# Performance work log

Hardware: AMD Instinct MI355X
Metric: run time of the kernel (lower is better)

The kernel has to match this reference:

```python
import jax, jax.numpy as jnp
import numpy as np

N = 8192
F_IN = 256
F_OUT = 256
S = 128          # state_dim
D_INNER = 512    # int(2.0 * out_features)


def _ln(x, g, b, eps=1e-5):
    m = x.mean(-1, keepdims=True)
    v = ((x - m) ** 2).mean(-1, keepdims=True)
    return (x - m) / jnp.sqrt(v + eps) * g + b


def setup_inputs() -> dict:
    key = jax.random.key(0)
    ks = jax.random.split(key, 20)
    s = 0.05
    d = {}
    d['h'] = jax.random.normal(ks[0], (N, F_IN), dtype=jnp.float32)
    d['adj'] = jax.random.randint(ks[1], (N, N), 0, 2, dtype=jnp.int32)
    d['W'] = jax.random.normal(ks[2], (F_IN, F_OUT), dtype=jnp.float32) * s
    d['a_src'] = jax.random.normal(ks[3], (F_OUT, 1), dtype=jnp.float32) * s
    d['a_dst'] = jax.random.normal(ks[4], (F_OUT, 1), dtype=jnp.float32) * s
    d['W_bcdt'] = jax.random.normal(ks[5], (F_OUT, 3 * S), dtype=jnp.float32) * s
    d['b_bcdt'] = jnp.zeros((3 * S,), jnp.float32)
    d['abp_w'] = jax.random.normal(ks[6], (S, F_OUT), dtype=jnp.float32) * s
    d['abp_b'] = jnp.zeros((F_OUT,), jnp.float32)
    d['cp_w'] = jax.random.normal(ks[7], (S, 1), dtype=jnp.float32) * s
    d['cp_b'] = jnp.zeros((1,), jnp.float32)
    d['W_hz'] = jax.random.normal(ks[8], (F_OUT, 2 * D_INNER), dtype=jnp.float32) * s
    d['b_hz'] = jnp.zeros((2 * D_INNER,), jnp.float32)
    d['out_w'] = jax.random.normal(ks[9], (D_INNER, F_OUT), dtype=jnp.float32) * s
    d['out_b'] = jnp.zeros((F_OUT,), jnp.float32)
    d['fe1_w'] = jax.random.normal(ks[10], (F_OUT, D_INNER), dtype=jnp.float32) * s
    d['fe1_b'] = jnp.zeros((D_INNER,), jnp.float32)
    d['fe_ln_g'] = jnp.ones((D_INNER,), jnp.float32)
    d['fe_ln_b'] = jnp.zeros((D_INNER,), jnp.float32)
    d['fe2_w'] = jax.random.normal(ks[11], (D_INNER, F_OUT), dtype=jnp.float32) * s
    d['fe2_b'] = jnp.zeros((F_OUT,), jnp.float32)
    d['A'] = jax.random.uniform(ks[12], (S,), minval=1.0, maxval=64.0, dtype=jnp.float32)
    d['D'] = jnp.ones((1,), jnp.float32)
    d['g1_w'] = jax.random.normal(ks[13], (2 * F_OUT, 2 * F_OUT), dtype=jnp.float32) * s
    d['g1_b'] = jnp.zeros((2 * F_OUT,), jnp.float32)
    d['g_ln_g'] = jnp.ones((2 * F_OUT,), jnp.float32)
    d['g_ln_b'] = jnp.zeros((2 * F_OUT,), jnp.float32)
    d['g2_w'] = jax.random.normal(ks[14], (2 * F_OUT, F_OUT), dtype=jnp.float32) * s
    d['g2_b'] = jnp.zeros((F_OUT,), jnp.float32)
    d['ln_g'] = jnp.ones((F_OUT,), jnp.float32)
    d['ln_b'] = jnp.zeros((F_OUT,), jnp.float32)
    return d


def reference(h, adj, W, a_src, a_dst, W_bcdt, b_bcdt, abp_w, abp_b, cp_w, cp_b,
              W_hz, b_hz, out_w, out_b, fe1_w, fe1_b, fe_ln_g, fe_ln_b, fe2_w,
              fe2_b, A, D, g1_w, g1_b, g_ln_g, g_ln_b, g2_w, g2_b, ln_g, ln_b):
    Wh = h @ W                                   # [N, F_OUT]
    # GAT-style masked attention
    e = Wh @ a_src + (Wh @ a_dst).T              # [N, N]
    e = jnp.where(e > 0, e, 0.2 * e)             # leaky_relu(0.2)
    e = jnp.where(adj > 0, e, jnp.float32(-9e15))
    attn = jax.nn.softmax(e, axis=1)
    h_attn = attn @ Wh                           # [N, F_OUT]
    # feature enhancer
    h_enh = jax.nn.silu(_ln(Wh @ fe1_w + fe1_b, fe_ln_g, fe_ln_b)) @ fe2_w + fe2_b
    # SSM-like branch
    BCdt = Wh @ W_bcdt + b_bcdt                  # [N, 3S]
    B, C, dt = jnp.split(BCdt, 3, axis=1)
    Asm = jax.nn.softmax(dt + A[None, :], axis=1)
    ab = (Asm * B) @ abp_w + abp_b               # [N, F_OUT]
    hs = Wh * ab
    hz = hs @ W_hz + b_hz                        # [N, 2*D_INNER]
    h_part, z = jnp.split(hz, 2, axis=1)
    hs = (h_part * jax.nn.silu(z) + h_part * D) @ out_w + out_b
    c_proj = C @ cp_w + cp_b                     # [N, 1]
    hs = hs * (1.0 + c_proj)
    # gated fusion
    comb = jnp.concatenate([h_attn, hs], axis=1)  # [N, 2*F_OUT]
    g = jax.nn.sigmoid(jax.nn.silu(_ln(comb @ g1_w + g1_b, g_ln_g, g_ln_b)) @ g2_w + g2_b)
    fused = g * h_attn + (1.0 - g) * hs + h_enh
    return _ln(fused, ln_g, ln_b)
```

## Files before the change

kernel.cpp:

```cpp
#include <hip/hip_runtime.h>
#include <cstdint>

typedef __attribute__((ext_vector_type(8))) short short8;
typedef __attribute__((ext_vector_type(4))) float f32x4;

#define DEVINL static __device__ __forceinline__

DEVINL ushort f2b(float f) {
    uint32_t u = __builtin_bit_cast(uint32_t, f);
    u += 0x7FFFu + ((u >> 16) & 1u);
    return (ushort)(u >> 16);
}

typedef __attribute__((address_space(3))) uint32_t lds_u32;
typedef const __attribute__((address_space(1))) uint32_t glb_u32;

DEVINL void load_lds_16(const ushort* g, ushort* l) {
    __builtin_amdgcn_global_load_lds((glb_u32*)g, (lds_u32*)l, 16, 0, 0);
}

constexpr int EPI_F32      = 0;
constexpr int EPI_MUL_BF16 = 2;
constexpr int EPI_SCALE_FB = 3;
constexpr int EPI_WH       = 4;

template<int K, int EPI>
__global__ __launch_bounds__(256) void gemm_k(
    const ushort* __restrict__ A, const ushort* __restrict__ BT,
    const float* __restrict__ bias, int N,
    float* __restrict__ outf, ushort* __restrict__ outb, int obld, int oboff,
    const float* __restrict__ extra,
    const float* __restrict__ asrc, const float* __restrict__ adst,
    float* __restrict__ sOut, float* __restrict__ dOut)
{
    __shared__ ushort Asm[128 * 64];
    __shared__ ushort Bsm[64 * 64];

    const int wave = threadIdx.x >> 6;
    const int lane = threadIdx.x & 63;
    const int quad = lane >> 4;
    const int l16  = lane & 15;
    const int lr   = lane >> 3, ls = lane & 7;
    const int m0 = blockIdx.x * 128;
    const int n0 = blockIdx.y * 64;

    f32x4 zero = {0.f, 0.f, 0.f, 0.f};
    f32x4 acc[2][4] = {{zero, zero, zero, zero}, {zero, zero, zero, zero}};

    for (int k0 = 0; k0 < K; k0 += 64) {
        #pragma unroll
        for (int p = 0; p < 4; ++p) {
            const int r = wave * 32 + p * 8 + lr;
            load_lds_16(A + (size_t)(m0 + r) * K + k0 + ((ls ^ (r & 7)) * 8),
                        Asm + (size_t)(wave * 32 + p * 8) * 64);
        }
        #pragma unroll
        for (int p = 0; p < 2; ++p) {
            const int n = wave * 16 + p * 8 + lr;
            load_lds_16(BT + (size_t)(n0 + n) * K + k0 + ((ls ^ (n & 7)) * 8),
                        Bsm + (size_t)(wave * 16 + p * 8) * 64);
        }
        __syncthreads();
        #pragma unroll
        for (int ks = 0; ks < 2; ++ks) {
            const int kg = ks * 4 + quad;
            const int sl = (kg ^ (l16 & 7)) * 8;
            short8 a0 = *(const short8*)(Asm + (wave * 32 + l16) * 64 + sl);
            short8 a1 = *(const short8*)(Asm + (wave * 32 + 16 + l16) * 64 + sl);
            #pragma unroll
            for (int c = 0; c < 4; ++c) {
                short8 bf = *(const short8*)(Bsm + (c * 16 + l16) * 64 + sl);
                acc[0][c] = __builtin_amdgcn_mfma_f32_16x16x32_bf16(a0, bf, acc[0][c], 0, 0, 0);
                acc[1][c] = __builtin_amdgcn_mfma_f32_16x16x32_bf16(a1, bf, acc[1][c], 0, 0, 0);
            }
        }
        __syncthreads();
    }

    #pragma unroll
    for (int it = 0; it < 2; ++it) {
        #pragma unroll
        for (int r = 0; r < 4; ++r) {
            const int row = m0 + wave * 32 + it * 16 + quad * 4 + r;
            float sp = 0.f, dp = 0.f;
            #pragma unroll
            for (int c = 0; c < 4; ++c) {
                const int col = n0 + c * 16 + l16;
                float v = acc[it][c][r] + (bias ? bias[col] : 0.f);
                if (EPI == EPI_MUL_BF16) v *= extra[(size_t)row * N + col];
                if (EPI == EPI_SCALE_FB) v *= extra[row];
                if (EPI == EPI_F32 || EPI == EPI_SCALE_FB || EPI == EPI_WH)
                    outf[(size_t)row * N + col] = v;
                if (EPI == EPI_MUL_BF16 || EPI == EPI_SCALE_FB || EPI == EPI_WH)
                    outb[(size_t)row * obld + oboff + col] = f2b(v);
                if (EPI == EPI_WH) { sp += v * asrc[col]; dp += v * adst[col]; }
            }
            if (EPI == EPI_WH) {
                #pragma unroll
                for (int o = 1; o < 16; o <<= 1) {
                    sp += __shfl_xor(sp, o);
                    dp += __shfl_xor(dp, o);
                }
                if (l16 == 0) {
                    atomicAdd(&sOut[row], sp);
                    atomicAdd(&dOut[row], dp);
                }
            }
        }
    }
}

__global__ __launch_bounds__(256) void attn_kernel(
    const int* __restrict__ adj, const float* __restrict__ sA,
    const float* __restrict__ dA, const ushort* __restrict__ WhT,
    float* __restrict__ Upart, float* __restrict__ lpart)
{
    __shared__ ushort vsm[256 * 64];
    __shared__ ushort wsm[64 * 64];

    const int tid  = threadIdx.x;
    const int wave = tid >> 6, lane = tid & 63, quad = lane >> 4, l16 = lane & 15;
    const int lr = lane >> 3, ls = lane & 7;
    const int i0 = blockIdx.x * 64;
    const int js = blockIdx.y;
    const int jbase = js * 2048;
    const int pr = tid >> 2, pc = tid & 3;
    const float s_r = sA[i0 + pr];
    const int* adjp = adj + (size_t)(i0 + pr) * 8192 + jbase;
    const int rt = wave & 1, ch = wave >> 1;

    f32x4 zero = {0.f, 0.f, 0.f, 0.f};
    f32x4 acc[2][8] = {{zero, zero, zero, zero, zero, zero, zero, zero},
                       {zero, zero, zero, zero, zero, zero, zero, zero}};
    float lsum = 0.f;

    for (int c64 = 0; c64 < 2048; c64 += 64) {
        #pragma unroll
        for (int p = 0; p < 8; ++p) {
            const int f = wave * 64 + p * 8 + lr;
            load_lds_16(WhT + (size_t)f * 8192 + jbase + c64 + ((ls ^ (f & 7)) * 8),
                        vsm + (size_t)(wave * 64 + p * 8) * 64);
        }
        #pragma unroll
        for (int gi = 0; gi < 2; ++gi) {
            const int g = pc + gi * 4;
            const int4   a0 = *(const int4*)  (adjp + c64 + g * 8);
            const int4   a1 = *(const int4*)  (adjp + c64 + g * 8 + 4);
            const float4 d0 = *(const float4*)(dA + jbase + c64 + g * 8);
            const float4 d1 = *(const float4*)(dA + jbase + c64 + g * 8 + 4);
            const int   aa[8] = {a0.x, a0.y, a0.z, a0.w, a1.x, a1.y, a1.z, a1.w};
            const float dd[8] = {d0.x, d0.y, d0.z, d0.w, d1.x, d1.y, d1.z, d1.w};
            union { ushort us[8]; uint4 v; } pk;
            #pragma unroll
            for (int q = 0; q < 8; ++q) {
                float e = s_r + dd[q];
                e = fmaxf(e, 0.2f * e);
                const float w = aa[q] ? __expf(e) : 0.f;
                lsum += w; pk.us[q] = f2b(w);
            }
            *(uint4*)(wsm + pr * 64 + ((g ^ (pr & 7)) * 8)) = pk.v;
        }
        __syncthreads();

        #pragma unroll
        for (int ks = 0; ks < 2; ++ks) {
            const int kg = ks * 4 + quad;
            const int sl = (kg ^ (l16 & 7)) * 8;
            short8 a0 = *(const short8*)(wsm + (rt * 32 + l16) * 64 + sl);
            short8 a1 = *(const short8*)(wsm + (rt * 32 + 16 + l16) * 64 + sl);
            #pragma unroll
            for (int c = 0; c < 8; ++c) {
                short8 bf = *(const short8*)(vsm + (ch * 128 + c * 16 + l16) * 64 + sl);
                acc[0][c] = __builtin_amdgcn_mfma_f32_16x16x32_bf16(a0, bf, acc[0][c], 0, 0, 0);
                acc[1][c] = __builtin_amdgcn_mfma_f32_16x16x32_bf16(a1, bf, acc[1][c], 0, 0, 0);
            }
        }
        __syncthreads();
    }

    lsum += __shfl_down(lsum, 1);
    lsum += __shfl_down(lsum, 2);
    if (pc == 0) lpart[(size_t)js * 8192 + i0 + pr] = lsum;

    #pragma unroll
    for (int it = 0; it < 2; ++it) {
        #pragma unroll
        for (int c = 0; c < 8; ++c) {
            const int col = ch * 128 + c * 16 + l16;
            #pragma unroll
            for (int r = 0; r < 4; ++r) {
                const int row = i0 + rt * 32 + it * 16 + quad * 4 + r;
                Upart[((size_t)js * 8192 + row) * 256 + col] = acc[it][c][r];
            }
        }
    }
}

__global__ __launch_bounds__(256) void attn_combine_kernel(
    const float* __restrict__ Upart, const float* __restrict__ lpart,
    float* __restrict__ outf, ushort* __restrict__ outb)
{
    const int row = blockIdx.x * 4 + (threadIdx.x >> 6);
    const int lane = threadIdx.x & 63;
    float l = 0.f;
    #pragma unroll
    for (int js = 0; js < 4; ++js) l += lpart[(size_t)js * 8192 + row];
    const float inv = 1.f / l;
    #pragma unroll
    for (int i = 0; i < 4; ++i) {
        const int c = i * 64 + lane;
        float u = 0.f;
        #pragma unroll
        for (int js = 0; js < 4; ++js)
            u += Upart[((size_t)js * 8192 + row) * 256 + c];
        const float v = u * inv;
        outf[(size_t)row * 256 + c] = v;
        outb[(size_t)row * 512 + c] = f2b(v);
    }
}

struct TJob { const float* in; ushort* out; int R, C, off; };
struct TArgs { TJob j[10]; };

__global__ __launch_bounds__(256) void multi_transpose_kernel(TArgs a)
{
    __shared__ float tile[32][33];
    const int b = blockIdx.x;
    int ji = 0;
    #pragma unroll
    for (int k = 1; k < 10; ++k) if (b >= a.j[k].off) ji = k;
    const TJob J = a.j[ji];
    const int t = b - J.off;

    if (J.R == 0) {
        const int base = t * 1024 + threadIdx.x;
        #pragma unroll
        for (int k = 0; k < 4; ++k)
            J.out[base + k * 256] = f2b(J.in[base + k * 256]);
        return;
    }
    const int CB = J.C >> 5;
    const int bx = t % CB, by = t / CB;
    const int tx = threadIdx.x & 31, ty = threadIdx.x >> 5;
    const int c0 = bx * 32, r0 = by * 32;
    #pragma unroll
    for (int i = ty; i < 32; i += 8)
        tile[i][tx] = J.in[(size_t)(r0 + i) * J.C + (c0 + tx)];
    __syncthreads();
    #pragma unroll
    for (int i = ty; i < 32; i += 8)
        J.out[(size_t)(c0 + i) * J.R + (r0 + tx)] = f2b(tile[tx][i]);
}

__global__ __launch_bounds__(256) void transpose_cast_kernel(
    const float* __restrict__ in, ushort* __restrict__ out, int R, int C)
{
    __shared__ float tile[32][33];
    const int tx = threadIdx.x & 31, ty = threadIdx.x >> 5;
    const int c0 = blockIdx.x * 32, r0 = blockIdx.y * 32;
    #pragma unroll
    for (int i = ty; i < 32; i += 8)
        tile[i][tx] = in[(size_t)(r0 + i) * C + (c0 + tx)];
    __syncthreads();
    #pragma unroll
    for (int i = ty; i < 32; i += 8)
        out[(size_t)(c0 + i) * R + (r0 + tx)] = f2b(tile[tx][i]);
}

__global__ __launch_bounds__(256) void ln_silu_512_kernel(
    const float* __restrict__ in, const float* __restrict__ g,
    const float* __restrict__ b, ushort* __restrict__ outb)
{
    const int row = blockIdx.x * 4 + (threadIdx.x >> 6);
    const int lane = threadIdx.x & 63;
    const size_t base = (size_t)row * 512;
    float x[8]; float sum = 0.f, sq = 0.f;
    #pragma unroll
    for (int i = 0; i < 8; ++i) {
        const float v = in[base + i * 64 + lane];
        x[i] = v; sum += v; sq += v * v;
    }
    #pragma unroll
    for (int o = 32; o; o >>= 1) { sum += __shfl_xor(sum, o); sq += __shfl_xor(sq, o); }
    const float mean = sum * (1.f / 512.f);
    const float var  = sq * (1.f / 512.f) - mean * mean;
    const float rstd = rsqrtf(var + 1e-5f);
    #pragma unroll
    for (int i = 0; i < 8; ++i) {
        const int c = i * 64 + lane;
        const float y = (x[i] - mean) * rstd * g[c] + b[c];
        outb[base + c] = f2b(y / (1.f + __expf(-y)));
    }
}

__global__ __launch_bounds__(256) void ssm_front_kernel(
    const float* __restrict__ BCdt, const float* __restrict__ Avec,
    const float* __restrict__ cpw, const float* __restrict__ cpb,
    ushort* __restrict__ SB, float* __restrict__ cscale)
{
    const int row = blockIdx.x * 4 + (threadIdx.x >> 6);
    const int lane = threadIdx.x & 63;
    const float* rp = BCdt + (size_t)row * 384;
    const float B0 = rp[lane],       B1 = rp[64 + lane];
    const float C0 = rp[128 + lane], C1 = rp[192 + lane];
    float t0 = rp[256 + lane] + Avec[lane];
    float t1 = rp[320 + lane] + Avec[64 + lane];
    float mx = fmaxf(t0, t1);
    #pragma unroll
    for (int o = 32; o; o >>= 1) mx = fmaxf(mx, __shfl_xor(mx, o));
    const float e0 = __expf(t0 - mx), e1 = __expf(t1 - mx);
    float ssum = e0 + e1;
    #pragma unroll
    for (int o = 32; o; o >>= 1) ssum += __shfl_xor(ssum, o);
    const float inv = 1.f / ssum;
    SB[(size_t)row * 128 + lane]      = f2b(e0 * inv * B0);
    SB[(size_t)row * 128 + 64 + lane] = f2b(e1 * inv * B1);
    float cp = C0 * cpw[lane] + C1 * cpw[64 + lane];
    #pragma unroll
    for (int o = 32; o; o >>= 1) cp += __shfl_xor(cp, o);
    if (lane == 0) cscale[row] = 1.f + cp + cpb[0];
}

__global__ void hz_act_kernel(const float* __restrict__ hz,
                              const float* __restrict__ Dp, ushort* __restrict__ out)
{
    const float D0 = Dp[0];
    const int n = 8192 * 512;
    for (int i = blockIdx.x * blockDim.x + threadIdx.x; i < n; i += gridDim.x * blockDim.x) {
        const int r = i >> 9, c = i & 511;
        const float hp = hz[(size_t)r * 1024 + c];
        const float z  = hz[(size_t)r * 1024 + 512 + c];
        out[i] = f2b(hp * (z / (1.f + __expf(-z)) + D0));
    }
}

__global__ __launch_bounds__(256) void final_kernel(
    const float* __restrict__ gl, const float* __restrict__ ha,
    const float* __restrict__ hs2, const float* __restrict__ he,
    const float* __restrict__ lng, const float* __restrict__ lnb,
    float* __restrict__ outp)
{
    const int row = blockIdx.x * 4 + (threadIdx.x >> 6);
    const int lane = threadIdx.x & 63;
    const size_t base = (size_t)row * 256;
    float f[4]; float sum = 0.f, sq = 0.f;
    #pragma unroll
    for (int i = 0; i < 4; ++i) {
        const int c = i * 64 + lane;
        const float gv = 1.f / (1.f + __expf(-gl[base + c]));
        const float v = gv * ha[base + c] + (1.f - gv) * hs2[base + c] + he[base + c];
        f[i] = v; sum += v; sq += v * v;
    }
    #pragma unroll
    for (int o = 32; o; o >>= 1) { sum += __shfl_xor(sum, o); sq += __shfl_xor(sq, o); }
    const float mean = sum * (1.f / 256.f);
    const float var  = sq * (1.f / 256.f) - mean * mean;
    const float rstd = rsqrtf(var + 1e-5f);
    #pragma unroll
    for (int i = 0; i < 4; ++i) {
        const int c = i * 64 + lane;
        outp[base + c] = (f[i] - mean) * rstd * lng[c] + lnb[c];
    }
}

extern "C" void kernel_launch(void* const* d_in, const int* in_sizes, int n_in,
                              void* d_out, int out_size, void* d_ws, size_t ws_size,
                              hipStream_t stream)
{
    const float* h      = (const float*)d_in[0];
    const int*   adj    = (const int*)  d_in[1];
    const float* W      = (const float*)d_in[2];
    const float* a_src  = (const float*)d_in[3];
    const float* a_dst  = (const float*)d_in[4];
    const float* W_bcdt = (const float*)d_in[5];
    const float* b_bcdt = (const float*)d_in[6];
    const float* abp_w  = (const float*)d_in[7];
    const float* abp_b  = (const float*)d_in[8];
    const float* cp_w   = (const float*)d_in[9];
    const float* cp_b   = (const float*)d_in[10];
    const float* W_hz   = (const float*)d_in[11];
    const float* b_hz   = (const float*)d_in[12];
    const float* out_w  = (const float*)d_in[13];
    const float* out_b  = (const float*)d_in[14];
    const float* fe1_w  = (const float*)d_in[15];
    const float* fe1_b  = (const float*)d_in[16];
    const float* fe_ln_g= (const float*)d_in[17];
    const float* fe_ln_b= (const float*)d_in[18];
    const float* fe2_w  = (const float*)d_in[19];
    const float* fe2_b  = (const float*)d_in[20];
    const float* Avec   = (const float*)d_in[21];
    const float* Dvec   = (const float*)d_in[22];
    const float* g1_w   = (const float*)d_in[23];
    const float* g1_b   = (const float*)d_in[24];
    const float* g_ln_g = (const float*)d_in[25];
    const float* g_ln_b = (const float*)d_in[26];
    const float* g2_w   = (const float*)d_in[27];
    const float* g2_b   = (const float*)d_in[28];
    const float* ln_g   = (const float*)d_in[29];
    const float* ln_b   = (const float*)d_in[30];
    float* outp = (float*)d_out;

    char* p = (char*)d_ws;
    size_t off = 0;
    auto take = [&](size_t nbytes) -> void* {
        void* r = p + off;
        off += (nbytes + 255) & ~(size_t)255;
        return r;
    };
    ushort* wT    = (ushort*)take(256 * 256 * 2);
    ushort* fe1T  = (ushort*)take(512 * 256 * 2);
    ushort* fe2T  = (ushort*)take(256 * 512 * 2);
    ushort* bcdtT = (ushort*)take(384 * 256 * 2);
    ushort* abpT  = (ushort*)take(256 * 128 * 2);
    ushort* hzT   = (ushort*)take(1024 * 256 * 2);
    ushort* outT  = (ushort*)take(256 * 512 * 2);
    ushort* g1T   = (ushort*)take(512 * 512 * 2);
    ushort* g2T   = (ushort*)take(256 * 512 * 2);
    ushort* hbf   = (ushort*)take((size_t)8192 * 256 * 2);
    float*  Wh    = (float*) take((size_t)8192 * 256 * 4);
    ushort* Whbf  = (ushort*)take((size_t)8192 * 256 * 2);
    ushort* WhT   = (ushort*)take((size_t)8192 * 256 * 2);
    float*  sbuf  = (float*) take(8192 * 4);
    float*  dbuf  = (float*) take(8192 * 4);
    float*  cscl  = (float*) take(8192 * 4);
    float*  hattn = (float*) take((size_t)8192 * 256 * 4);
    float*  henh  = (float*) take((size_t)8192 * 256 * 4);
    float*  BCdt  = (float*) take((size_t)8192 * 384 * 4);
    ushort* SB    = (ushort*)take((size_t)8192 * 128 * 2);
    ushort* hsbf  = (ushort*)take((size_t)8192 * 256 * 2);
    ushort* vbf   = (ushort*)take((size_t)8192 * 512 * 2);
    float*  hs2   = (float*) take((size_t)8192 * 256 * 4);
    ushort* comb  = (ushort*)take((size_t)8192 * 512 * 2);
    ushort* tact  = (ushort*)take((size_t)8192 * 512 * 2);
    float*  big   = (float*) take((size_t)8192 * 1024 * 4);
    float*  gl    = BCdt;
    float*  Upart = big;
    float*  lpart = BCdt;

    (void)in_sizes; (void)n_in; (void)out_size; (void)ws_size;

    hipMemsetAsync(sbuf, 0, 2 * 8192 * sizeof(float), stream);

    {
        TArgs ta; int boff = 0;
        auto addT = [&](int i, const float* in, ushort* out, int R, int C) {
            ta.j[i] = TJob{in, out, R, C, boff};
            boff += (R / 32) * (C / 32);
        };
        addT(0, W,      wT,    256, 256);
        addT(1, fe1_w,  fe1T,  256, 512);
        addT(2, fe2_w,  fe2T,  512, 256);
        addT(3, W_bcdt, bcdtT, 256, 384);
        addT(4, abp_w,  abpT,  128, 256);
        addT(5, W_hz,   hzT,   256, 1024);
        addT(6, out_w,  outT,  512, 256);
        addT(7, g1_w,   g1T,   512, 512);
        addT(8, g2_w,   g2T,   512, 256);
        ta.j[9] = TJob{h, hbf, 0, 8192 * 256, boff};
        boff += (8192 * 256) / 1024;
        multi_transpose_kernel<<<boff, 256, 0, stream>>>(ta);
    }

    gemm_k<256, EPI_WH><<<dim3(64, 4), 256, 0, stream>>>(
        hbf, wT, nullptr, 256, Wh, Whbf, 256, 0, nullptr, a_src, a_dst, sbuf, dbuf);
    transpose_cast_kernel<<<dim3(8, 256), 256, 0, stream>>>(Wh, WhT, 8192, 256);

    attn_kernel<<<dim3(128, 4), 256, 0, stream>>>(adj, sbuf, dbuf, WhT, Upart, lpart);
    attn_combine_kernel<<<2048, 256, 0, stream>>>(Upart, lpart, hattn, comb);

    gemm_k<256, EPI_F32><<<dim3(64, 8), 256, 0, stream>>>(
        Whbf, fe1T, fe1_b, 512, big, nullptr, 0, 0, nullptr, nullptr, nullptr, nullptr, nullptr);
    ln_silu_512_kernel<<<2048, 256, 0, stream>>>(big, fe_ln_g, fe_ln_b, tact);
    gemm_k<512, EPI_F32><<<dim3(64, 4), 256, 0, stream>>>(
        tact, fe2T, fe2_b, 256, henh, nullptr, 0, 0, nullptr, nullptr, nullptr, nullptr, nullptr);

    gemm_k<256, EPI_F32><<<dim3(64, 6), 256, 0, stream>>>(
        Whbf, bcdtT, b_bcdt, 384, BCdt, nullptr, 0, 0, nullptr, nullptr, nullptr, nullptr, nullptr);
    ssm_front_kernel<<<2048, 256, 0, stream>>>(BCdt, Avec, cp_w, cp_b, SB, cscl);
    gemm_k<128, EPI_MUL_BF16><<<dim3(64, 4), 256, 0, stream>>>(
        SB, abpT, abp_b, 256, nullptr, hsbf, 256, 0, Wh, nullptr, nullptr, nullptr, nullptr);
    gemm_k<256, EPI_F32><<<dim3(64, 16), 256, 0, stream>>>(
        hsbf, hzT, b_hz, 1024, big, nullptr, 0, 0, nullptr, nullptr, nullptr, nullptr, nullptr);
    hz_act_kernel<<<4096, 256, 0, stream>>>(big, Dvec, vbf);
    gemm_k<512, EPI_SCALE_FB><<<dim3(64, 4), 256, 0, stream>>>(
        vbf, outT, out_b, 256, hs2, comb, 512, 256, cscl, nullptr, nullptr, nullptr, nullptr);

    gemm_k<512, EPI_F32><<<dim3(64, 8), 256, 0, stream>>>(
        comb, g1T, g1_b, 512, big, nullptr, 0, 0, nullptr, nullptr, nullptr, nullptr, nullptr);
    ln_silu_512_kernel<<<2048, 256, 0, stream>>>(big, g_ln_g, g_ln_b, tact);
    gemm_k<512, EPI_F32><<<dim3(64, 4), 256, 0, stream>>>(
        tact, g2T, g2_b, 256, gl, nullptr, 0, 0, nullptr, nullptr, nullptr, nullptr, nullptr);
    final_kernel<<<2048, 256, 0, stream>>>(gl, hattn, hs2, henh, ln_g, ln_b, outp);
}
```

Baseline: 645.9 us.

## Fuse row-wise epilogues (LN+SiLU, SSM softmax, hz gating, final LN) into GEMMs

Adds a full-row GEMM kernel with 16-row tiles spanning all output columns, so LayerNorm+SiLU, the SSM softmax/scale, the hz gating and the final gated-fusion LayerNorm run in the GEMM epilogue. This drops the separate elementwise kernels and the fp32 intermediate round trips through global memory. The W_hz weight columns are permuted during transpose so each block holds matching h and z halves. The generic GEMM tile is halved to 64x64 to double the grid. Small row tiles reload the whole B matrix per block and get less reuse, and the attention scratch buffers are now separately allocated.

```diff
diff --git a/kernel.cpp b/kernel.cpp
--- a/kernel.cpp
+++ b/kernel.cpp
@@ -33,78 +33,313 @@
     const float* __restrict__ asrc, const float* __restrict__ adst,
     float* __restrict__ sOut, float* __restrict__ dOut)
 {
-    __shared__ ushort Asm[128 * 64];
+    __shared__ ushort Asm[64 * 64];
     __shared__ ushort Bsm[64 * 64];
 
     const int wave = threadIdx.x >> 6;
     const int lane = threadIdx.x & 63;
-    const int quad = lane >> 4;
-    const int l16  = lane & 15;
-    const int lr   = lane >> 3, ls = lane & 7;
-    const int m0 = blockIdx.x * 128;
+    const int quad = lane >> 4, l16 = lane & 15;
+    const int lr = lane >> 3, ls = lane & 7;
+    const int m0 = blockIdx.x * 64;
     const int n0 = blockIdx.y * 64;
 
     f32x4 zero = {0.f, 0.f, 0.f, 0.f};
-    f32x4 acc[2][4] = {{zero, zero, zero, zero}, {zero, zero, zero, zero}};
+    f32x4 acc[4] = {zero, zero, zero, zero};
 
     for (int k0 = 0; k0 < K; k0 += 64) {
         #pragma unroll
-        for (int p = 0; p < 4; ++p) {
-            const int r = wave * 32 + p * 8 + lr;
+        for (int p = 0; p < 2; ++p) {
+            const int r = wave * 16 + p * 8 + lr;
             load_lds_16(A + (size_t)(m0 + r) * K + k0 + ((ls ^ (r & 7)) * 8),
-                        Asm + (size_t)(wave * 32 + p * 8) * 64);
-        }
-        #pragma unroll
-        for (int p = 0; p < 2; ++p) {
-            const int n = wave * 16 + p * 8 + lr;
-            load_lds_16(BT + (size_t)(n0 + n) * K + k0 + ((ls ^ (n & 7)) * 8),
+                        Asm + (size_t)(wave * 16 + p * 8) * 64);
+            load_lds_16(BT + (size_t)(n0 + r) * K + k0 + ((ls ^ (r & 7)) * 8),
                         Bsm + (size_t)(wave * 16 + p * 8) * 64);
         }
         __syncthreads();
         #pragma unroll
         for (int ks = 0; ks < 2; ++ks) {
-            const int kg = ks * 4 + quad;
-            const int sl = (kg ^ (l16 & 7)) * 8;
-            short8 a0 = *(const short8*)(Asm + (wave * 32 + l16) * 64 + sl);
-            short8 a1 = *(const short8*)(Asm + (wave * 32 + 16 + l16) * 64 + sl);
+            const int sl = ((ks * 4 + quad) ^ (l16 & 7)) * 8;
+            short8 af = *(const short8*)(Asm + (wave * 16 + l16) * 64 + sl);
             #pragma unroll
             for (int c = 0; c < 4; ++c) {
                 short8 bf = *(const short8*)(Bsm + (c * 16 + l16) * 64 + sl);
-                acc[0][c] = __builtin_amdgcn_mfma_f32_16x16x32_bf16(a0, bf, acc[0][c], 0, 0, 0);
-                acc[1][c] = __builtin_amdgcn_mfma_f32_16x16x32_bf16(a1, bf, acc[1][c], 0, 0, 0);
-            }
-        }
-        __syncthreads();
-    }
-
-    #pragma unroll
-    for (int it = 0; it < 2; ++it) {
-        #pragma unroll
-        for (int r = 0; r < 4; ++r) {
-            const int row = m0 + wave * 32 + it * 16 + quad * 4 + r;
-            float sp = 0.f, dp = 0.f;
-            #pragma unroll
-            for (int c = 0; c < 4; ++c) {
-                const int col = n0 + c * 16 + l16;
-                float v = acc[it][c][r] + (bias ? bias[col] : 0.f);
-                if (EPI == EPI_MUL_BF16) v *= extra[(size_t)row * N + col];
-                if (EPI == EPI_SCALE_FB) v *= extra[row];
-                if (EPI == EPI_F32 || EPI == EPI_SCALE_FB || EPI == EPI_WH)
-                    outf[(size_t)row * N + col] = v;
-                if (EPI == EPI_MUL_BF16 || EPI == EPI_SCALE_FB || EPI == EPI_WH)
-                    outb[(size_t)row * obld + oboff + col] = f2b(v);
-                if (EPI == EPI_WH) { sp += v * asrc[col]; dp += v * adst[col]; }
-            }
-            if (EPI == EPI_WH) {
+                acc[c] = __builtin_amdgcn_mfma_f32_16x16x32_bf16(af, bf, acc[c], 0, 0, 0);
+            }
+        }
+        __syncthreads();
+    }
+
+    #pragma unroll
+    for (int r = 0; r < 4; ++r) {
+        const int row = m0 + wave * 16 + quad * 4 + r;
+        float sp = 0.f, dp = 0.f;
+        #pragma unroll
+        for (int c = 0; c < 4; ++c) {
+            const int col = n0 + c * 16 + l16;
+            float v = acc[c][r] + (bias ? bias[col] : 0.f);
+            if (EPI == EPI_MUL_BF16) v *= extra[(size_t)row * N + col];
+            if (EPI == EPI_SCALE_FB) v *= extra[row];
+            if (EPI == EPI_F32 || EPI == EPI_SCALE_FB || EPI == EPI_WH)
+                outf[(size_t)row * N + col] = v;
+            if (EPI == EPI_MUL_BF16 || EPI == EPI_SCALE_FB || EPI == EPI_WH)
+                outb[(size_t)row * obld + oboff + col] = f2b(v);
+            if (EPI == EPI_WH) { sp += v * asrc[col]; dp += v * adst[col]; }
+        }
+        if (EPI == EPI_WH) {
+            #pragma unroll
+            for (int o = 1; o < 16; o <<= 1) {
+                sp += __shfl_xor(sp, o);
+                dp += __shfl_xor(dp, o);
+            }
+            if (l16 == 0) {
+                atomicAdd(&sOut[row], sp);
+                atomicAdd(&dOut[row], dp);
+            }
+        }
+    }
+}
+
+constexpr int EPR_LNSILU = 0;
+constexpr int EPR_BCDT   = 1;
+constexpr int EPR_HZ     = 2;
+constexpr int EPR_FINAL  = 3;
+
+template<int K, int N, int EPI>
+__global__ __launch_bounds__(256) void gemm_row(
+    const ushort* __restrict__ A, const ushort* __restrict__ BT,
+    const float* __restrict__ bias,
+    float* __restrict__ outf, ushort* __restrict__ outb,
+    const float* __restrict__ q0, const float* __restrict__ q1,
+    const float* __restrict__ q2, const float* __restrict__ q3,
+    const float* __restrict__ q4)
+{
+    constexpr int NW = N / 4;
+    constexpr int NF = NW / 16;
+    __shared__ ushort Asm[16 * 64];
+    __shared__ ushort Bsm[N * 64];
+    __shared__ float red[192];
+
+    const int wave = threadIdx.x >> 6;
+    const int lane = threadIdx.x & 63;
+    const int quad = lane >> 4, l16 = lane & 15;
+    const int lr = lane >> 3, ls = lane & 7;
+    const int m0 = blockIdx.x * 16;
+    const ushort* Bb = BT + (EPI == EPR_HZ ? (size_t)blockIdx.y * 512 * K : 0);
+
+    f32x4 zero = {0.f, 0.f, 0.f, 0.f};
+    f32x4 acc[NF];
+    #pragma unroll
+    for (int c = 0; c < NF; ++c) acc[c] = zero;
+
+    for (int k0 = 0; k0 < K; k0 += 64) {
+        if (wave < 2) {
+            const int r = wave * 8 + lr;
+            load_lds_16(A + (size_t)(m0 + r) * K + k0 + ((ls ^ (r & 7)) * 8),
+                        Asm + (size_t)(wave * 8) * 64);
+        }
+        #pragma unroll
+        for (int p = 0; p < NW / 8; ++p) {
+            const int n = wave * NW + p * 8 + lr;
+            load_lds_16(Bb + (size_t)n * K + k0 + ((ls ^ (n & 7)) * 8),
+                        Bsm + (size_t)(wave * NW + p * 8) * 64);
+        }
+        __syncthreads();
+        #pragma unroll
+        for (int ks = 0; ks < 2; ++ks) {
+            const int sl = ((ks * 4 + quad) ^ (l16 & 7)) * 8;
+            short8 af = *(const short8*)(Asm + l16 * 64 + sl);
+            #pragma unroll
+            for (int c = 0; c < NF; ++c) {
+                const int gf = (EPI == EPR_BCDT) ? (wave + 4 * c) : (wave * NF + c);
+                short8 bf = *(const short8*)(Bsm + (gf * 16 + l16) * 64 + sl);
+                acc[c] = __builtin_amdgcn_mfma_f32_16x16x32_bf16(af, bf, acc[c], 0, 0, 0);
+            }
+        }
+        __syncthreads();
+    }
+
+    if constexpr (EPI != EPR_HZ) {
+        #pragma unroll
+        for (int c = 0; c < NF; ++c) {
+            const int gf = (EPI == EPR_BCDT) ? (wave + 4 * c) : (wave * NF + c);
+            const float bs = bias[gf * 16 + l16];
+            #pragma unroll
+            for (int r = 0; r < 4; ++r) acc[c][r] += bs;
+        }
+    }
+
+    if constexpr (EPI == EPR_LNSILU) {
+        float s[4], q[4];
+        #pragma unroll
+        for (int r = 0; r < 4; ++r) {
+            s[r] = 0.f; q[r] = 0.f;
+            #pragma unroll
+            for (int c = 0; c < NF; ++c) { const float v = acc[c][r]; s[r] += v; q[r] += v * v; }
+            #pragma unroll
+            for (int o = 1; o < 16; o <<= 1) { s[r] += __shfl_xor(s[r], o); q[r] += __shfl_xor(q[r], o); }
+        }
+        if (l16 == 0) {
+            #pragma unroll
+            for (int r = 0; r < 4; ++r) {
+                red[(quad * 4 + r) * 8 + wave * 2]     = s[r];
+                red[(quad * 4 + r) * 8 + wave * 2 + 1] = q[r];
+            }
+        }
+        __syncthreads();
+        #pragma unroll
+        for (int r = 0; r < 4; ++r) {
+            const int row16 = quad * 4 + r;
+            float S = 0.f, Q = 0.f;
+            #pragma unroll
+            for (int w = 0; w < 4; ++w) { S += red[row16 * 8 + w * 2]; Q += red[row16 * 8 + w * 2 + 1]; }
+            const float mean = S * (1.f / N);
+            const float rstd = rsqrtf(Q * (1.f / N) - mean * mean + 1e-5f);
+            #pragma unroll
+            for (int c = 0; c < NF; ++c) {
+                const int col = (wave * NF + c) * 16 + l16;
+                const float y = (acc[c][r] - mean) * rstd * q0[col] + q1[col];
+                outb[(size_t)(m0 + row16) * N + col] = f2b(y / (1.f + __expf(-y)));
+            }
+        }
+    } else if constexpr (EPI == EPR_BCDT) {
+        float t[2][4], e[2][4];
+        #pragma unroll
+        for (int ci = 0; ci < 2; ++ci) {
+            const int dcol = (wave + 4 * (ci + 4)) * 16 - 256 + l16;
+            const float av = q0[dcol];
+            #pragma unroll
+            for (int r = 0; r < 4; ++r) t[ci][r] = acc[ci + 4][r] + av;
+        }
+        float pm[4];
+        #pragma unroll
+        for (int r = 0; r < 4; ++r) {
+            pm[r] = fmaxf(t[0][r], t[1][r]);
+            #pragma unroll
+            for (int o = 1; o < 16; o <<= 1) pm[r] = fmaxf(pm[r], __shfl_xor(pm[r], o));
+        }
+        if (l16 == 0) {
+            #pragma unroll
+            for (int r = 0; r < 4; ++r) red[(quad * 4 + r) * 4 + wave] = pm[r];
+        }
+        __syncthreads();
+        float mx[4];
+        #pragma unroll
+        for (int r = 0; r < 4; ++r) {
+            const int row16 = quad * 4 + r;
+            mx[r] = fmaxf(fmaxf(red[row16 * 4], red[row16 * 4 + 1]),
+                          fmaxf(red[row16 * 4 + 2], red[row16 * 4 + 3]));
+        }
+        float pe[4], pc[4];
+        #pragma unroll
+        for (int r = 0; r < 4; ++r) {
+            e[0][r] = __expf(t[0][r] - mx[r]);
+            e[1][r] = __expf(t[1][r] - mx[r]);
+            pe[r] = e[0][r] + e[1][r];
+            pc[r] = 0.f;
+            #pragma unroll
+            for (int ci = 0; ci < 2; ++ci) {
+                const int ccol = (wave + 4 * (ci + 2)) * 16 - 128 + l16;
+                pc[r] += acc[ci + 2][r] * q1[ccol];
+            }
+            #pragma unroll
+            for (int o = 1; o < 16; o <<= 1) { pe[r] += __shfl_xor(pe[r], o); pc[r] += __shfl_xor(pc[r], o); }
+        }
+        if (l16 == 0) {
+            #pragma unroll
+            for (int r = 0; r < 4; ++r) {
+                red[64  + (quad * 4 + r) * 4 + wave] = pe[r];
+                red[128 + (quad * 4 + r) * 4 + wave] = pc[r];
+            }
+        }
+        __syncthreads();
+        #pragma unroll
+        for (int r = 0; r < 4; ++r) {
+            const int row16 = quad * 4 + r;
+            const float inv = 1.f / (red[64 + row16 * 4] + red[64 + row16 * 4 + 1] +
+                                     red[64 + row16 * 4 + 2] + red[64 + row16 * 4 + 3]);
+            #pragma unroll
+            for (int ci = 0; ci < 2; ++ci) {
+                const int bcol = (wave + 4 * ci) * 16 + l16;
+                outb[(size_t)(m0 + row16) * 128 + bcol] = f2b(acc[ci][r] * e[ci][r] * inv);
+            }
+        }
+        if (wave == 0 && l16 == 0) {
+            #pragma unroll
+            for (int r = 0; r < 4; ++r) {
+                const int row16 = quad * 4 + r;
+                outf[m0 + row16] = 1.f + red[128 + row16 * 4] + red[128 + row16 * 4 + 1] +
+                                   red[128 + row16 * 4 + 2] + red[128 + row16 * 4 + 3] + q2[0];
+            }
+        }
+    } else if constexpr (EPI == EPR_HZ) {
+        float* ep = (float*)Bsm;
+        const float D0 = q0[0];
+        const int y = blockIdx.y;
+        if (wave >= 2) {
+            #pragma unroll
+            for (int c = 0; c < NF; ++c) {
+                const int lc = (wave * NF + c) * 16 + l16;
+                const float bz = bias[512 + y * 256 + lc - 256];
                 #pragma unroll
-                for (int o = 1; o < 16; o <<= 1) {
-                    sp += __shfl_xor(sp, o);
-                    dp += __shfl_xor(dp, o);
+                for (int r = 0; r < 4; ++r) {
+                    const float z = acc[c][r] + bz;
+                    ep[(quad * 4 + r) * 256 + lc - 256] = z / (1.f + __expf(-z)) + D0;
                 }
-                if (l16 == 0) {
-                    atomicAdd(&sOut[row], sp);
-                    atomicAdd(&dOut[row], dp);
+            }
+        }
+        __syncthreads();
+        if (wave < 2) {
+            #pragma unroll
+            for (int c = 0; c < NF; ++c) {
+                const int lc = (wave * NF + c) * 16 + l16;
+                const float bh = bias[y * 256 + lc];
+                #pragma unroll
+                for (int r = 0; r < 4; ++r) {
+                    const float v = (acc[c][r] + bh) * ep[(quad * 4 + r) * 256 + lc];
+                    outb[(size_t)(m0 + quad * 4 + r) * 512 + y * 256 + lc] = f2b(v);
                 }
+            }
+        }
+    } else {
+        float fv[4][4], s[4], q[4];
+        #pragma unroll
+        for (int r = 0; r < 4; ++r) { s[r] = 0.f; q[r] = 0.f; }
+        #pragma unroll
+        for (int c = 0; c < NF; ++c) {
+            const int col = (wave * NF + c) * 16 + l16;
+            #pragma unroll
+            for (int r = 0; r < 4; ++r) {
+                const size_t idx = (size_t)(m0 + quad * 4 + r) * 256 + col;
+                const float g = 1.f / (1.f + __expf(-acc[c][r]));
+                const float f = g * q0[idx] + (1.f - g) * q1[idx] + q2[idx];
+                fv[c][r] = f; s[r] += f; q[r] += f * f;
+            }
+        }
+        #pragma unroll
+        for (int r = 0; r < 4; ++r) {
+            #pragma unroll
+            for (int o = 1; o < 16; o <<= 1) { s[r] += __shfl_xor(s[r], o); q[r] += __shfl_xor(q[r], o); }
+        }
+        if (l16 == 0) {
+            #pragma unroll
+            for (int r = 0; r < 4; ++r) {
+                red[(quad * 4 + r) * 8 + wave * 2]     = s[r];
+                red[(quad * 4 + r) * 8 + wave * 2 + 1] = q[r];
+            }
+        }
+        __syncthreads();
+        #pragma unroll
+        for (int r = 0; r < 4; ++r) {
+            const int row16 = quad * 4 + r;
+            float S = 0.f, Q = 0.f;
+            #pragma unroll
+            for (int w = 0; w < 4; ++w) { S += red[row16 * 8 + w * 2]; Q += red[row16 * 8 + w * 2 + 1]; }
+            const float mean = S * (1.f / 256.f);
+            const float rstd = rsqrtf(Q * (1.f / 256.f) - mean * mean + 1e-5f);
+            #pragma unroll
+            for (int c = 0; c < NF; ++c) {
+                const int col = (wave * NF + c) * 16 + l16;
+                outf[(size_t)(m0 + row16) * 256 + col] = (fv[c][r] - mean) * rstd * q3[col] + q4[col];
             }
         }
     }
@@ -164,8 +399,7 @@
 
         #pragma unroll
         for (int ks = 0; ks < 2; ++ks) {
-            const int kg = ks * 4 + quad;
-            const int sl = (kg ^ (l16 & 7)) * 8;
+            const int sl = ((ks * 4 + quad) ^ (l16 & 7)) * 8;
             short8 a0 = *(const short8*)(wsm + (rt * 32 + l16) * 64 + sl);
             short8 a1 = *(const short8*)(wsm + (rt * 32 + 16 + l16) * 64 + sl);
             #pragma unroll
@@ -219,8 +453,13 @@
     }
 }
 
-struct TJob { const float* in; ushort* out; int R, C, off; };
+struct TJob { const float* in; ushort* out; int R, C, off, perm; };
 struct TArgs { TJob j[10]; };
+
+DEVINL int hzperm(int j) {
+    return (j < 512) ? ((j >> 8) << 9) + (j & 255)
+                     : (((j - 512) >> 8) << 9) + 256 + ((j - 512) & 255);
+}
 
 __global__ __launch_bounds__(256) void multi_transpose_kernel(TArgs a)
 {
@@ -248,8 +487,11 @@
         tile[i][tx] = J.in[(size_t)(r0 + i) * J.C + (c0 + tx)];
     __syncthreads();
     #pragma unroll
-    for (int i = ty; i < 32; i += 8)
-        J.out[(size_t)(c0 + i) * J.R + (r0 + tx)] = f2b(tile[tx][i]);
+    for (int i = ty; i < 32; i += 8) {
+        int orow = c0 + i;
+        if (J.perm) orow = hzperm(orow);
+        J.out[(size_t)orow * J.R + (r0 + tx)] = f2b(tile[tx][i]);
+    }
 }
 
 __global__ __launch_bounds__(256) void transpose_cast_kernel(
@@ -265,102 +507,6 @@
     #pragma unroll
     for (int i = ty; i < 32; i += 8)
         out[(size_t)(c0 + i) * R + (r0 + tx)] = f2b(tile[tx][i]);
-}
-
-__global__ __launch_bounds__(256) void ln_silu_512_kernel(
-    const float* __restrict__ in, const float* __restrict__ g,
-    const float* __restrict__ b, ushort* __restrict__ outb)
-{
-    const int row = blockIdx.x * 4 + (threadIdx.x >> 6);
-    const int lane = threadIdx.x & 63;
-    const size_t base = (size_t)row * 512;
-    float x[8]; float sum = 0.f, sq = 0.f;
-    #pragma unroll
-    for (int i = 0; i < 8; ++i) {
-        const float v = in[base + i * 64 + lane];
-        x[i] = v; sum += v; sq += v * v;
-    }
-    #pragma unroll
-    for (int o = 32; o; o >>= 1) { sum += __shfl_xor(sum, o); sq += __shfl_xor(sq, o); }
-    const float mean = sum * (1.f / 512.f);
-    const float var  = sq * (1.f / 512.f) - mean * mean;
-    const float rstd = rsqrtf(var + 1e-5f);
-    #pragma unroll
-    for (int i = 0; i < 8; ++i) {
-        const int c = i * 64 + lane;
-        const float y = (x[i] - mean) * rstd * g[c] + b[c];
-        outb[base + c] = f2b(y / (1.f + __expf(-y)));
-    }
-}
-
-__global__ __launch_bounds__(256) void ssm_front_kernel(
-    const float* __restrict__ BCdt, const float* __restrict__ Avec,
-    const float* __restrict__ cpw, const float* __restrict__ cpb,
-    ushort* __restrict__ SB, float* __restrict__ cscale)
-{
-    const int row = blockIdx.x * 4 + (threadIdx.x >> 6);
-    const int lane = threadIdx.x & 63;
-    const float* rp = BCdt + (size_t)row * 384;
-    const float B0 = rp[lane],       B1 = rp[64 + lane];
-    const float C0 = rp[128 + lane], C1 = rp[192 + lane];
-    float t0 = rp[256 + lane] + Avec[lane];
-    float t1 = rp[320 + lane] + Avec[64 + lane];
-    float mx = fmaxf(t0, t1);
-    #pragma unroll
-    for (int o = 32; o; o >>= 1) mx = fmaxf(mx, __shfl_xor(mx, o));
-    const float e0 = __expf(t0 - mx), e1 = __expf(t1 - mx);
-    float ssum = e0 + e1;
-    #pragma unroll
-    for (int o = 32; o; o >>= 1) ssum += __shfl_xor(ssum, o);
-    const float inv = 1.f / ssum;
-    SB[(size_t)row * 128 + lane]      = f2b(e0 * inv * B0);
-    SB[(size_t)row * 128 + 64 + lane] = f2b(e1 * inv * B1);
-    float cp = C0 * cpw[lane] + C1 * cpw[64 + lane];
-    #pragma unroll
-    for (int o = 32; o; o >>= 1) cp += __shfl_xor(cp, o);
-    if (lane == 0) cscale[row] = 1.f + cp + cpb[0];
-}
-
-__global__ void hz_act_kernel(const float* __restrict__ hz,
-                              const float* __restrict__ Dp, ushort* __restrict__ out)
-{
-    const float D0 = Dp[0];
-    const int n = 8192 * 512;
-    for (int i = blockIdx.x * blockDim.x + threadIdx.x; i < n; i += gridDim.x * blockDim.x) {
-        const int r = i >> 9, c = i & 511;
-        const float hp = hz[(size_t)r * 1024 + c];
-        const float z  = hz[(size_t)r * 1024 + 512 + c];
-        out[i] = f2b(hp * (z / (1.f + __expf(-z)) + D0));
-    }
-}
-
-__global__ __launch_bounds__(256) void final_kernel(
-    const float* __restrict__ gl, const float* __restrict__ ha,
-    const float* __restrict__ hs2, const float* __restrict__ he,
-    const float* __restrict__ lng, const float* __restrict__ lnb,
-    float* __restrict__ outp)
-{
-    const int row = blockIdx.x * 4 + (threadIdx.x >> 6);
-    const int lane = threadIdx.x & 63;
-    const size_t base = (size_t)row * 256;
-    float f[4]; float sum = 0.f, sq = 0.f;
-    #pragma unroll
-    for (int i = 0; i < 4; ++i) {
-        const int c = i * 64 + lane;
-        const float gv = 1.f / (1.f + __expf(-gl[base + c]));
-        const float v = gv * ha[base + c] + (1.f - gv) * hs2[base + c] + he[base + c];
-        f[i] = v; sum += v; sq += v * v;
-    }
-    #pragma unroll
-    for (int o = 32; o; o >>= 1) { sum += __shfl_xor(sum, o); sq += __shfl_xor(sq, o); }
-    const float mean = sum * (1.f / 256.f);
-    const float var  = sq * (1.f / 256.f) - mean * mean;
-    const float rstd = rsqrtf(var + 1e-5f);
-    #pragma unroll
-    for (int i = 0; i < 4; ++i) {
-        const int c = i * 64 + lane;
-        outp[base + c] = (f[i] - mean) * rstd * lng[c] + lnb[c];
-    }
 }
 
 extern "C" void kernel_launch(void* const* d_in, const int* in_sizes, int n_in,
@@ -411,11 +557,11 @@
     ushort* fe1T  = (ushort*)take(512 * 256 * 2);
     ushort* fe2T  = (ushort*)take(256 * 512 * 2);
     ushort* bcdtT = (ushort*)take(384 * 256 * 2);
-    ushort* abpT  = (ushort*)take(256 * 128 * 2);
     ushort* hzT   = (ushort*)take(1024 * 256 * 2);
     ushort* outT  = (ushort*)take(256 * 512 * 2);
     ushort* g1T   = (ushort*)take(512 * 512 * 2);
     ushort* g2T   = (ushort*)take(256 * 512 * 2);
+    ushort* abpT  = (ushort*)take(256 * 128 * 2);
     ushort* hbf   = (ushort*)take((size_t)8192 * 256 * 2);
     float*  Wh    = (float*) take((size_t)8192 * 256 * 4);
     ushort* Whbf  = (ushort*)take((size_t)8192 * 256 * 2);
@@ -425,17 +571,14 @@
     float*  cscl  = (float*) take(8192 * 4);
     float*  hattn = (float*) take((size_t)8192 * 256 * 4);
     float*  henh  = (float*) take((size_t)8192 * 256 * 4);
-    float*  BCdt  = (float*) take((size_t)8192 * 384 * 4);
+    float*  lpart = (float*) take(4 * 8192 * 4);
     ushort* SB    = (ushort*)take((size_t)8192 * 128 * 2);
     ushort* hsbf  = (ushort*)take((size_t)8192 * 256 * 2);
     ushort* vbf   = (ushort*)take((size_t)8192 * 512 * 2);
     float*  hs2   = (float*) take((size_t)8192 * 256 * 4);
     ushort* comb  = (ushort*)take((size_t)8192 * 512 * 2);
     ushort* tact  = (ushort*)take((size_t)8192 * 512 * 2);
-    float*  big   = (float*) take((size_t)8192 * 1024 * 4);
-    float*  gl    = BCdt;
-    float*  Upart = big;
-    float*  lpart = BCdt;
+    float*  Upart = (float*) take((size_t)4 * 8192 * 256 * 4);
 
     (void)in_sizes; (void)n_in; (void)out_size; (void)ws_size;
 
@@ -443,52 +586,47 @@
 
     {
         TArgs ta; int boff = 0;
-        auto addT = [&](int i, const float* in, ushort* out, int R, int C) {
-            ta.j[i] = TJob{in, out, R, C, boff};
+        auto addT = [&](int i, const float* in, ushort* out, int R, int C, int perm) {
+            ta.j[i] = TJob{in, out, R, C, boff, perm};
             boff += (R / 32) * (C / 32);
         };
-        addT(0, W,      wT,    256, 256);
-        addT(1, fe1_w,  fe1T,  256, 512);
-        addT(2, fe2_w,  fe2T,  512, 256);
-        addT(3, W_bcdt, bcdtT, 256, 384);
-        addT(4, abp_w,  abpT,  128, 256);
-        addT(5, W_hz,   hzT,   256, 1024);
-        addT(6, out_w,  outT,  512, 256);
-        addT(7, g1_w,   g1T,   512, 512);
-        addT(8, g2_w,   g2T,   512, 256);
-        ta.j[9] = TJob{h, hbf, 0, 8192 * 256, boff};
+        addT(0, W,      wT,    256, 256,  0);
+        addT(1, fe1_w,  fe1T,  256, 512,  0);
+        addT(2, fe2_w,  fe2T,  512, 256,  0);
+        addT(3, W_bcdt, bcdtT, 256, 384,  0);
+        addT(4, abp_w,  abpT,  128, 256,  0);
+        addT(5, W_hz,   hzT,   256, 1024, 1);
+        addT(6, out_w,  outT,  512, 256,  0);
+        addT(7, g1_w,   g1T,   512, 512,  0);
+        addT(8, g2_w,   g2T,   512, 256,  0);
+        ta.j[9] = TJob{h, hbf, 0, 8192 * 256, boff, 0};
         boff += (8192 * 256) / 1024;
         multi_transpose_kernel<<<boff, 256, 0, stream>>>(ta);
     }
 
-    gemm_k<256, EPI_WH><<<dim3(64, 4), 256, 0, stream>>>(
+    gemm_k<256, EPI_WH><<<dim3(128, 4), 256, 0, stream>>>(
         hbf, wT, nullptr, 256, Wh, Whbf, 256, 0, nullptr, a_src, a_dst, sbuf, dbuf);
     transpose_cast_kernel<<<dim3(8, 256), 256, 0, stream>>>(Wh, WhT, 8192, 256);
 
     attn_kernel<<<dim3(128, 4), 256, 0, stream>>>(adj, sbuf, dbuf, WhT, Upart, lpart);
     attn_combine_kernel<<<2048, 256, 0, stream>>>(Upart, lpart, hattn, comb);
 
-    gemm_k<256, EPI_F32><<<dim3(64, 8), 256, 0, stream>>>(
-        Whbf, fe1T, fe1_b, 512, big, nullptr, 0, 0, nullptr, nullptr, nullptr, nullptr, nullptr);
-    ln_silu_512_kernel<<<2048, 256, 0, stream>>>(big, fe_ln_g, fe_ln_b, tact);
-    gemm_k<512, EPI_F32><<<dim3(64, 4), 256, 0, stream>>>(
+    gemm_row<256, 512, EPR_LNSILU><<<512, 256, 0, stream>>>(
+        Whbf, fe1T, fe1_b, nullptr, tact, fe_ln_g, fe_ln_b, nullptr, nullptr, nullptr);
+    gemm_k<512, EPI_F32><<<dim3(128, 4), 256, 0, stream>>>(
         tact, fe2T, fe2_b, 256, henh, nullptr, 0, 0, nullptr, nullptr, nullptr, nullptr, nullptr);
 
-    gemm_k<256, EPI_F32><<<dim3(64, 6), 256, 0, stream>>>(
-        Whbf, bcdtT, b_bcdt, 384, BCdt, nullptr, 0, 0, nullptr, nullptr, nullptr, nullptr, nullptr);
-    ssm_front_kernel<<<2048, 256, 0, stream>>>(BCdt, Avec, cp_w, cp_b, SB, cscl);
-    gemm_k<128, EPI_MUL_BF16><<<dim3(64, 4), 256, 0, stream>>>(
+    gemm_row<256, 384, EPR_BCDT><<<512, 256, 0, stream>>>(
+        Whbf, bcdtT, b_bcdt, cscl, SB, Avec, cp_w, cp_b, nullptr, nullptr);
+    gemm_k<128, EPI_MUL_BF16><<<dim3(128, 4), 256, 0, stream>>>(
         SB, abpT, abp_b, 256, nullptr, hsbf, 256, 0, Wh, nullptr, nullptr, nullptr, nullptr);
-    gemm_k<256, EPI_F32><<<dim3(64, 16), 256, 0, stream>>>(
-        hsbf, hzT, b_hz, 1024, big, nullptr, 0, 0, nullptr, nullptr, nullptr, nullptr, nullptr);
-    hz_act_kernel<<<4096, 256, 0, stream>>>(big, Dvec, vbf);
-    gemm_k<512, EPI_SCALE_FB><<<dim3(64, 4), 256, 0, stream>>>(
+    gemm_row<256, 512, EPR_HZ><<<dim3(512, 2), 256, 0, stream>>>(
+        hsbf, hzT, b_hz, nullptr, vbf, Dvec, nullptr, nullptr, nullptr, nullptr);
+    gemm_k<512, EPI_SCALE_FB><<<dim3(128, 4), 256, 0, stream>>>(
         vbf, outT, out_b, 256, hs2, comb, 512, 256, cscl, nullptr, nullptr, nullptr, nullptr);
 
-    gemm_k<512, EPI_F32><<<dim3(64, 8), 256, 0, stream>>>(
-        comb, g1T, g1_b, 512, big, nullptr, 0, 0, nullptr, nullptr, nullptr, nullptr, nullptr);
-    ln_silu_512_kernel<<<2048, 256, 0, stream>>>(big, g_ln_g, g_ln_b, tact);
-    gemm_k<512, EPI_F32><<<dim3(64, 4), 256, 0, stream>>>(
-        tact, g2T, g2_b, 256, gl, nullptr, 0, 0, nullptr, nullptr, nullptr, nullptr, nullptr);
-    final_kernel<<<2048, 256, 0, stream>>>(gl, hattn, hs2, henh, ln_g, ln_b, outp);
-}
+    gemm_row<512, 512, EPR_LNSILU><<<512, 256, 0, stream>>>(
+        comb, g1T, g1_b, nullptr, tact, g_ln_g, g_ln_b, nullptr, nullptr, nullptr);
+    gemm_row<512, 256, EPR_FINAL><<<512, 256, 0, stream>>>(
+        tact, g2T, g2_b, outp, nullptr, hattn, hs2, henh, ln_g, ln_b);
+}
```

New measurement: 611.2 us. -5.4%, faster.
